# Kernel tuning notes

Measured on AMD Instinct MI355X. Metric: run time of the kernel, lower is better.

## Reference

```python
import jax, jax.numpy as jnp
import numpy as np

N_NODES = 100000
N_EDGES = 3200000
NUM_FEATURES = 1433
HIDDEN = 16
NUM_CLASSES = 7


def setup_inputs() -> dict:
    key = jax.random.key(0)
    k1, k2, k3, k4, k5, k6 = jax.random.split(key, 6)
    x = jax.random.normal(k1, (N_NODES, NUM_FEATURES), dtype=jnp.float32)
    edge_index = jax.random.randint(k2, (2, N_EDGES), 0, N_NODES, dtype=jnp.int64)
    # Glorot-ish init for the two GCN layer weights + zero biases
    W1 = jax.random.normal(k3, (NUM_FEATURES, HIDDEN), dtype=jnp.float32) / np.sqrt(NUM_FEATURES)
    b1 = jnp.zeros((HIDDEN,), dtype=jnp.float32)
    W2 = jax.random.normal(k4, (HIDDEN, NUM_CLASSES), dtype=jnp.float32) / np.sqrt(HIDDEN)
    b2 = jnp.zeros((NUM_CLASSES,), dtype=jnp.float32)
    return {"x": x, "edge_index": edge_index, "W1": W1, "b1": b1, "W2": W2, "b2": b2}


def _gcn_conv(x, W, b, src, dst, deg_inv_sqrt, n_nodes):
    # PyG GCNConv: h = D^{-1/2}(A+I)D^{-1/2} (x W) + b
    h = x @ W                                   # [N, out]
    coef = deg_inv_sqrt[src] * deg_inv_sqrt[dst]  # [E]
    msg = h[src] * coef[:, None]                # gather + scale, [E, out]
    agg = jax.ops.segment_sum(msg, dst, num_segments=n_nodes)  # scatter-add
    return agg + b


def reference(x, edge_index, W1, b1, W2, b2):
    n = x.shape[0]
    loops = jnp.arange(n, dtype=edge_index.dtype)
    src = jnp.concatenate([edge_index[0], loops])  # add self-loops
    dst = jnp.concatenate([edge_index[1], loops])
    deg = jax.ops.segment_sum(jnp.ones_like(dst, dtype=x.dtype), dst, num_segments=n)
    deg_inv_sqrt = jnp.where(deg > 0, jax.lax.rsqrt(deg), 0.0)

    h = _gcn_conv(x, W1, b1, src, dst, deg_inv_sqrt, n)
    h = jax.nn.relu(h)
    h = _gcn_conv(h, W2, b2, src, dst, deg_inv_sqrt, n)
    h = jax.nn.relu(h)
    return jax.nn.log_softmax(h, axis=1)
```

## Files before the change

### kernel.cpp

```cpp
#include <hip/hip_runtime.h>
#include <hip/hip_bf16.h>
#include <math.h>

#define NF 1433
#define NH 16
#define NC 7
#define NCH 45
#define NBKT_MAX 1024
#define SC_C 3072
#define CAP 4608
#define SMASK 0x1FFFFFFu

typedef __attribute__((ext_vector_type(8))) short bf16x8;
typedef __attribute__((ext_vector_type(4))) float f32x4;

__device__ __forceinline__ unsigned short f2bf(float f) {
  unsigned int u = __float_as_uint(f);
  unsigned int r = (u + 0x7FFFu + ((u >> 16) & 1u)) >> 16;
  return (unsigned short)r;
}
__device__ __forceinline__ short f2bfs(float f) {
  union { __hip_bfloat16 h; short s; } u;
  u.h = __float2bfloat16(f);
  return u.s;
}
__device__ __forceinline__ unsigned int packbf(float lo, float hi) {
  return (unsigned int)f2bf(lo) | ((unsigned int)f2bf(hi) << 16);
}
__device__ __forceinline__ void acc8(float* a, uint4 r) {
  a[0] += __uint_as_float(r.x << 16); a[1] += __uint_as_float(r.x & 0xffff0000u);
  a[2] += __uint_as_float(r.y << 16); a[3] += __uint_as_float(r.y & 0xffff0000u);
  a[4] += __uint_as_float(r.z << 16); a[5] += __uint_as_float(r.z & 0xffff0000u);
  a[6] += __uint_as_float(r.w << 16); a[7] += __uint_as_float(r.w & 0xffff0000u);
}
__device__ __forceinline__ void acc8f(float* a, uint4 r, float c) {
  a[0] = fmaf(__uint_as_float(r.x << 16), c, a[0]);
  a[1] = fmaf(__uint_as_float(r.x & 0xffff0000u), c, a[1]);
  a[2] = fmaf(__uint_as_float(r.y << 16), c, a[2]);
  a[3] = fmaf(__uint_as_float(r.y & 0xffff0000u), c, a[3]);
  a[4] = fmaf(__uint_as_float(r.z << 16), c, a[4]);
  a[5] = fmaf(__uint_as_float(r.z & 0xffff0000u), c, a[5]);
  a[6] = fmaf(__uint_as_float(r.w << 16), c, a[6]);
  a[7] = fmaf(__uint_as_float(r.w & 0xffff0000u), c, a[7]);
}

#define GLOAD(gp, lp) __builtin_amdgcn_global_load_lds(                     \
    (const __attribute__((address_space(1))) void*)(gp),                    \
    (__attribute__((address_space(3))) void*)(lp), 4, 0, 0)

__global__ void k_prep(const float* __restrict__ W1, short* __restrict__ Wb,
                       int* __restrict__ bfill) {
  int t = blockIdx.x * blockDim.x + threadIdx.x;
  if (t < NBKT_MAX) bfill[t * 16] = t * CAP;
  if (t >= NCH * 64 * 8) return;
  int i = t & 7, l = (t >> 3) & 63, c = t >> 9;
  int g = l >> 4, col = l & 15;
  int k = c * 32 + g * 8 + i;
  float v = (k < NF) ? W1[(size_t)k * NH + col] : 0.f;
  Wb[t] = (short)f2bf(v);
}

__global__ __launch_bounds__(256) void k_fused(
    const float* __restrict__ x, const short* __restrict__ Wb,
    const int* __restrict__ ei, int* __restrict__ bfill,
    int* __restrict__ ebuf, unsigned short* __restrict__ hs1,
    int n, int E, int nbkt, int nsb) {
  __shared__ __align__(16) char smem[49664];
  int blk = blockIdx.x, t = threadIdx.x;
  int q = blk / 7, r7 = blk % 7;
  bool is_scatter = (r7 == 0) && (q < nsb);

  if (is_scatter) {
    int* h   = (int*)smem;
    int* lo  = h + NBKT_MAX;
    int* lb  = lo + NBKT_MAX;
    int* wtot = lb + NBKT_MAX;
    int* sval = wtot + 8;
    unsigned short* sbkt = (unsigned short*)(sval + SC_C);
    const int* src = ei;
    const int* dst = ei + E;
    for (int i = t; i < NBKT_MAX; i += 256) h[i] = 0;
    __syncthreads();
    int e0 = q * SC_C;
    int e1 = min(E, e0 + SC_C);
    int csize = e1 - e0;
    for (int e = e0 + t; e < e1; e += 256)
      atomicAdd(&h[((unsigned)dst[e]) >> 7], 1);
    __syncthreads();
    {
      int lane = t & 63, wvq = t >> 6;
      int v0 = h[4 * t], v1 = h[4 * t + 1], v2 = h[4 * t + 2], v3 = h[4 * t + 3];
      int s4 = v0 + v1 + v2 + v3;
      int inc = s4;
#pragma unroll
      for (int o = 1; o < 64; o <<= 1) {
        int u = __shfl_up(inc, o, 64);
        if (lane >= o) inc += u;
      }
      if (lane == 63) wtot[wvq] = inc;
      __syncthreads();
      int wbase = 0;
#pragma unroll
      for (int wq = 0; wq < 4; ++wq) wbase += (wq < wvq) ? wtot[wq] : 0;
      int base = wbase + inc - s4;
      lo[4 * t]     = base;
      lo[4 * t + 1] = base + v0;
      lo[4 * t + 2] = base + v0 + v1;
      lo[4 * t + 3] = base + v0 + v1 + v2;
    }
    __syncthreads();
    for (int i = t; i < nbkt; i += 256) {
      int c = h[i];
      lb[i] = c ? atomicAdd(&bfill[i * 16], c) : 0;
      h[i] = 0;
    }
    __syncthreads();
    for (int e = e0 + t; e < e1; e += 256) {
      unsigned d = (unsigned)dst[e];
      int bk = d >> 7;
      int p = lo[bk] + atomicAdd(&h[bk], 1);
      sval[p] = (int)(((d & 127u) << 25) | (unsigned)src[e]);
      sbkt[p] = (unsigned short)bk;
    }
    __syncthreads();
    for (int i = t; i < csize; i += 256) {
      int bk = sbkt[i];
      ebuf[lb[bk] + (i - lo[bk])] = sval[i];
    }
    return;
  }

  int gemm_id = blk - min((blk + 6) / 7, nsb);
  float* xsf = (float*)smem;
#define XIDX(B, ROW, COL) ((((B) * 16 + (ROW)) * 388) + (COL))
  int l = t & 63, wv = t >> 6;
  int row0 = gemm_id << 4;
  int rl = l & 15, g = l >> 4;

  const bf16x8* wp = (const bf16x8*)Wb + l;
  f32x4 acc;
#pragma unroll
  for (int j = 0; j < 4; ++j) acc[j] = 0.f;

  const float* rp[4];
#pragma unroll
  for (int r = 0; r < 4; ++r) {
    int row = row0 + 4 * wv + r;
    rp[r] = x + (size_t)((row < n) ? row : (n - 1)) * NF;
  }

#define STAGE6(M0, B) do {                                                   \
    _Pragma("unroll") for (int r = 0; r < 4; ++r)                            \
    _Pragma("unroll") for (int j = 0; j < 6; ++j)                            \
      GLOAD(rp[r] + (M0) + j * 64 + l, xsf + XIDX(B, 4 * wv + r, j * 64));   \
  } while (0)

#define DOCHUNK(B, CC, WREG) do {                                            \
    const float4* p = (const float4*)(xsf + XIDX(B, rl, (CC) * 32 + g * 8)); \
    float4 a0 = p[0], a1 = p[1];                                             \
    bf16x8 af;                                                               \
    af[0] = f2bfs(a0.x); af[1] = f2bfs(a0.y);                                \
    af[2] = f2bfs(a0.z); af[3] = f2bfs(a0.w);                                \
    af[4] = f2bfs(a1.x); af[5] = f2bfs(a1.y);                                \
    af[6] = f2bfs(a1.z); af[7] = f2bfs(a1.w);                                \
    acc = __builtin_amdgcn_mfma_f32_16x16x32_bf16(af, WREG, acc, 0, 0, 0);   \
  } while (0)

  STAGE6(0, 0);
  bf16x8 w0 = wp[(size_t)(wv) * 64];
  bf16x8 w1 = wp[(size_t)(wv + 4) * 64];
  bf16x8 w2 = wp[(size_t)(wv + 8) * 64];
  STAGE6(384, 1);
  asm volatile("s_waitcnt vmcnt(24) lgkmcnt(0)" ::: "memory");
  __builtin_amdgcn_s_barrier();
  DOCHUNK(0, wv, w0); DOCHUNK(0, wv + 4, w1); DOCHUNK(0, wv + 8, w2);
  __builtin_amdgcn_s_barrier();
  w0 = wp[(size_t)(12 + wv) * 64];
  w1 = wp[(size_t)(16 + wv) * 64];
  w2 = wp[(size_t)(20 + wv) * 64];
  STAGE6(768, 0);
  asm volatile("s_waitcnt vmcnt(24) lgkmcnt(0)" ::: "memory");
  __builtin_amdgcn_s_barrier();
  DOCHUNK(1, wv, w0); DOCHUNK(1, wv + 4, w1); DOCHUNK(1, wv + 8, w2);
  __builtin_amdgcn_s_barrier();
  w0 = wp[(size_t)(24 + wv) * 64];
  w1 = wp[(size_t)(28 + wv) * 64];
  w2 = wp[(size_t)(32 + wv) * 64];
#pragma unroll
  for (int r = 0; r < 4; ++r) {
#pragma unroll
    for (int j = 0; j < 4; ++j)
      GLOAD(rp[r] + 1152 + j * 64 + l, xsf + XIDX(1, 4 * wv + r, j * 64));
    GLOAD(rp[r] + (NF - 64) + l, xsf + XIDX(1, 4 * wv + r, 217));
  }
  if (l < 28) xsf[XIDX(1, 4 * wv + (l / 7), 281 + (l % 7))] = 0.f;
  asm volatile("s_waitcnt vmcnt(20) lgkmcnt(0)" ::: "memory");
  __builtin_amdgcn_s_barrier();
  DOCHUNK(0, wv, w0); DOCHUNK(0, wv + 4, w1); DOCHUNK(0, wv + 8, w2);
  __builtin_amdgcn_s_barrier();
  w0 = wp[(size_t)(36 + wv) * 64];
  w1 = wp[(size_t)(40 + wv) * 64];
  bf16x8 w2b = wp[(size_t)44 * 64];
  asm volatile("s_waitcnt vmcnt(0) lgkmcnt(0)" ::: "memory");
  __builtin_amdgcn_s_barrier();
  DOCHUNK(1, wv, w0); DOCHUNK(1, wv + 4, w1);
  if (wv == 0) DOCHUNK(1, 8, w2b);
  __syncthreads();

  float* ps = xsf;
#pragma unroll
  for (int r = 0; r < 4; ++r)
    ps[(wv * 16 + g * 4 + r) * 16 + rl] = acc[r];
  __syncthreads();
  if (wv == 0) {
    int row = l >> 2, c0 = (l & 3) * 4;
    float4 s0 = *(const float4*)&ps[(row) * 16 + c0];
    float4 s1 = *(const float4*)&ps[(16 + row) * 16 + c0];
    float4 s2 = *(const float4*)&ps[(32 + row) * 16 + c0];
    float4 s3 = *(const float4*)&ps[(48 + row) * 16 + c0];
    int grow = row0 + row;
    if (grow < n) {
      ushort4 o;
      o.x = f2bf(s0.x + s1.x + s2.x + s3.x);
      o.y = f2bf(s0.y + s1.y + s2.y + s3.y);
      o.z = f2bf(s0.z + s1.z + s2.z + s3.z);
      o.w = f2bf(s0.w + s1.w + s2.w + s3.w);
      *(ushort4*)(hs1 + (size_t)grow * NH + c0) = o;
    }
  }
#undef STAGE6
#undef DOCHUNK
#undef XIDX
}

__global__ __launch_bounds__(256) void k_bcsr(const int* __restrict__ ebuf,
                                              const int* __restrict__ bfill,
                                              int* __restrict__ off,
                                              int* __restrict__ end,
                                              int* __restrict__ srcs,
                                              float* __restrict__ dis, int n) {
  __shared__ int s_in[CAP];
  __shared__ int s_out[CAP];
  __shared__ int s_cnt[256];
  __shared__ int s_sc[256];
  int b = blockIdx.x, t = threadIdx.x;
  int eb = b * CAP;
  int cnt = bfill[b * 16] - eb;
  int cnt4 = cnt >> 2;

  const int4* e4 = (const int4*)(ebuf + eb);
  for (int i = t; i < cnt4; i += 256) ((int4*)s_in)[i] = e4[i];
  for (int i = cnt4 * 4 + t; i < cnt; i += 256) s_in[i] = ebuf[eb + i];
  s_cnt[t] = 0;
  __syncthreads();
  for (int i = t; i < cnt; i += 256)
    atomicAdd(&s_cnt[((unsigned)s_in[i]) >> 25], 1);
  __syncthreads();
  int deg = s_cnt[t];
  s_sc[t] = deg;
  __syncthreads();
  for (int o = 1; o < 256; o <<= 1) {
    int u = (t >= o) ? s_sc[t - o] : 0;
    __syncthreads();
    s_sc[t] += u;
    __syncthreads();
  }
  int excl = s_sc[t] - deg;
  int node = (b << 7) + t;
  if (t < 128 && node < n) {
    off[node] = eb + excl;
    end[node] = eb + excl + deg;
    dis[node] = rsqrtf((float)deg + 1.0f);
  }
  __syncthreads();
  s_cnt[t] = excl;
  __syncthreads();
  for (int i = t; i < cnt; i += 256) {
    unsigned v = (unsigned)s_in[i];
    int slot = atomicAdd(&s_cnt[v >> 25], 1);
    s_out[slot] = (int)(v & SMASK);
  }
  __syncthreads();
  int4* sr4 = (int4*)(srcs + eb);
  for (int i = t; i < cnt4; i += 256) sr4[i] = ((int4*)s_out)[i];
  for (int i = cnt4 * 4 + t; i < cnt; i += 256) srcs[eb + i] = s_out[i];
}

__global__ __launch_bounds__(256) void k_pull1(
    const int* __restrict__ off, const int* __restrict__ end,
    const int* __restrict__ srcs, const float* __restrict__ dis,
    const uint4* __restrict__ hs1, const float* __restrict__ b1,
    const float* __restrict__ W2, uint4* __restrict__ hs2, int n) {
  int t = blockIdx.x * blockDim.x + threadIdx.x;
  int d = t >> 4;
  if (d >= n) return;
  int sub = t & 15, half = sub & 1, ph = sub >> 1;
  float dd = dis[d];

  float a[8] = {0.f, 0.f, 0.f, 0.f, 0.f, 0.f, 0.f, 0.f};
  if (ph == 0) acc8f(a, hs1[(size_t)d * 2 + half], dd);

  int k = off[d] + ph, k1 = end[d];
  for (; k + 8 < k1; k += 16) {
    int s0 = srcs[k], s1 = srcs[k + 8];
    float c0 = dis[s0], c1 = dis[s1];
    uint4 r0 = hs1[(size_t)s0 * 2 + half];
    uint4 r1 = hs1[(size_t)s1 * 2 + half];
    acc8f(a, r0, c0);
    acc8f(a, r1, c1);
  }
  if (k < k1) {
    int s = srcs[k];
    acc8f(a, hs1[(size_t)s * 2 + half], dis[s]);
  }

#pragma unroll
  for (int i = 0; i < 8; ++i) {
    a[i] += __shfl_xor(a[i], 2);
    a[i] += __shfl_xor(a[i], 4);
    a[i] += __shfl_xor(a[i], 8);
  }

  float v[8];
#pragma unroll
  for (int i = 0; i < 8; ++i) v[i] = fmaxf(a[i] * dd + b1[half * 8 + i], 0.f);
  float p[NC];
#pragma unroll
  for (int c = 0; c < NC; ++c) {
    float s = 0.f;
#pragma unroll
    for (int i = 0; i < 8; ++i) s = fmaf(v[i], W2[(half * 8 + i) * NC + c], s);
    p[c] = s;
  }
#pragma unroll
  for (int c = 0; c < NC; ++c) p[c] += __shfl_xor(p[c], 1);
  if (sub == 0) {
    uint4 o;
    o.x = packbf(p[0] * dd, p[1] * dd);
    o.y = packbf(p[2] * dd, p[3] * dd);
    o.z = packbf(p[4] * dd, p[5] * dd);
    o.w = packbf(p[6] * dd, 0.f);
    hs2[d] = o;
  }
}

__global__ __launch_bounds__(256) void k_pull2(
    const int* __restrict__ off, const int* __restrict__ end,
    const int* __restrict__ srcs, const float* __restrict__ dis,
    const uint4* __restrict__ hs2, const float* __restrict__ b2,
    float* __restrict__ out, int n) {
  int t = blockIdx.x * blockDim.x + threadIdx.x;
  int d = t >> 3;
  if (d >= n) return;
  int ph = t & 7;

  float a[8] = {0.f, 0.f, 0.f, 0.f, 0.f, 0.f, 0.f, 0.f};
  if (ph == 0) acc8(a, hs2[d]);

  int k = off[d] + ph, k1 = end[d];
  for (; k + 8 < k1; k += 16) {
    int s0 = srcs[k], s1 = srcs[k + 8];
    uint4 r0 = hs2[s0];
    uint4 r1 = hs2[s1];
    acc8(a, r0);
    acc8(a, r1);
  }
  if (k < k1) acc8(a, hs2[srcs[k]]);

#pragma unroll
  for (int i = 0; i < 8; ++i) {
    a[i] += __shfl_xor(a[i], 1);
    a[i] += __shfl_xor(a[i], 2);
    a[i] += __shfl_xor(a[i], 4);
  }
  float dd = dis[d];
  float u[NC];
#pragma unroll
  for (int c = 0; c < NC; ++c) u[c] = fmaxf(a[c] * dd + b2[c], 0.f);
  float m = u[0];
#pragma unroll
  for (int c = 1; c < NC; ++c) m = fmaxf(m, u[c]);
  float sum = 0.f;
#pragma unroll
  for (int c = 0; c < NC; ++c) sum += expf(u[c] - m);
  float lg = logf(sum);
  if (ph < NC) out[(size_t)d * NC + ph] = u[ph] - m - lg;
}

extern "C" void kernel_launch(void* const* d_in, const int* in_sizes, int n_in,
                              void* d_out, int out_size, void* d_ws, size_t ws_size,
                              hipStream_t stream) {
  const float* x  = (const float*)d_in[0];
  const int*   ei = (const int*)d_in[1];
  const float* W1 = (const float*)d_in[2];
  const float* b1 = (const float*)d_in[3];
  const float* W2 = (const float*)d_in[4];
  const float* b2 = (const float*)d_in[5];
  int n = in_sizes[0] / NF;
  int E = in_sizes[1] / 2;
  int nbkt = (n + 127) >> 7;

  char* w = (char*)d_ws;
#define TAKE(ptrty, name, bytes) \
  ptrty name = (ptrty)w; w += ((size_t)(bytes) + 15) & ~(size_t)15;
  TAKE(unsigned short*, hs1,  sizeof(short) * (size_t)n * NH)
  TAKE(uint4*,          hs2,  16 * (size_t)n)
  TAKE(float*,          dis,  sizeof(float) * n)
  TAKE(short*,          Wb,   sizeof(short) * NCH * 64 * 8)
  TAKE(int*,            bfill,sizeof(int) * 16 * NBKT_MAX)
  TAKE(int*,            ebuf, sizeof(int) * (size_t)NBKT_MAX * CAP)
  TAKE(int*,            off,  sizeof(int) * n)
  TAKE(int*,            end,  sizeof(int) * n)
  TAKE(int*,            srcs, sizeof(int) * (size_t)NBKT_MAX * CAP)
#undef TAKE
  float* out = (float*)d_out;

  int nsb = (E + SC_C - 1) / SC_C;
  int ntb = (n + 15) / 16;

  k_prep<<<(NCH * 64 * 8 + 255) / 256, 256, 0, stream>>>(W1, Wb, bfill);

  k_fused<<<nsb + ntb, 256, 0, stream>>>(x, Wb, ei, bfill, ebuf, hs1,
                                         n, E, nbkt, nsb);

  k_bcsr<<<nbkt, 256, 0, stream>>>(ebuf, bfill, off, end, srcs, dis, n);
  k_pull1<<<((size_t)n * 16 + 255) / 256, 256, 0, stream>>>(
      off, end, srcs, dis, (const uint4*)hs1, b1, W2, hs2, n);
  k_pull2<<<((size_t)n * 8 + 255) / 256, 256, 0, stream>>>(
      off, end, srcs, dis, hs2, b2, out, n);
}
```

Baseline: 235.9 us.

## Fuse bucket-CSR build into fused kernel with atomic completion counter

Moves the per-bucket CSR construction (k_bcsr) into trailing blocks of k_fused. Those blocks spin on a global done counter that each scatter block increments after writing its edges. The aim is to drop a kernel launch and let the CSR build overlap with the tail of the GEMM blocks. It relies on the scatter blocks being scheduled before the waiting blocks, which holds because of block ordering, and spinning blocks may hold CU slots while the GEMM is still running.

```diff
diff --git a/kernel.cpp b/kernel.cpp
--- a/kernel.cpp
+++ b/kernel.cpp
@@ -49,9 +49,10 @@
     (__attribute__((address_space(3))) void*)(lp), 4, 0, 0)
 
 __global__ void k_prep(const float* __restrict__ W1, short* __restrict__ Wb,
-                       int* __restrict__ bfill) {
+                       int* __restrict__ bfill, int* __restrict__ done) {
   int t = blockIdx.x * blockDim.x + threadIdx.x;
   if (t < NBKT_MAX) bfill[t * 16] = t * CAP;
+  if (t < 16) done[t] = 0;
   if (t >= NCH * 64 * 8) return;
   int i = t & 7, l = (t >> 3) & 63, c = t >> 9;
   int g = l >> 4, col = l & 15;
@@ -64,9 +65,67 @@
     const float* __restrict__ x, const short* __restrict__ Wb,
     const int* __restrict__ ei, int* __restrict__ bfill,
     int* __restrict__ ebuf, unsigned short* __restrict__ hs1,
-    int n, int E, int nbkt, int nsb) {
+    int* __restrict__ off, int* __restrict__ end, int* __restrict__ srcs,
+    float* __restrict__ dis, int* __restrict__ done,
+    int n, int E, int nbkt, int nsb, int ntb) {
   __shared__ __align__(16) char smem[49664];
   int blk = blockIdx.x, t = threadIdx.x;
+
+  if (blk >= nsb + ntb) {
+    int b = blk - nsb - ntb;
+    int* s_in  = (int*)smem;
+    int* s_out = s_in + CAP;
+    int* s_cnt = s_out + CAP;
+    int* s_sc  = s_cnt + 256;
+    if (t == 0) {
+      while (__hip_atomic_load(done, __ATOMIC_ACQUIRE,
+                               __HIP_MEMORY_SCOPE_AGENT) < nsb)
+        __builtin_amdgcn_s_sleep(32);
+    }
+    __syncthreads();
+
+    int eb = b * CAP;
+    int cnt = bfill[b * 16] - eb;
+    int cnt4 = cnt >> 2;
+    const int4* e4 = (const int4*)(ebuf + eb);
+    for (int i = t; i < cnt4; i += 256) ((int4*)s_in)[i] = e4[i];
+    for (int i = cnt4 * 4 + t; i < cnt; i += 256) s_in[i] = ebuf[eb + i];
+    s_cnt[t] = 0;
+    __syncthreads();
+    for (int i = t; i < cnt; i += 256)
+      atomicAdd(&s_cnt[((unsigned)s_in[i]) >> 25], 1);
+    __syncthreads();
+    int deg = s_cnt[t];
+    s_sc[t] = deg;
+    __syncthreads();
+    for (int o = 1; o < 256; o <<= 1) {
+      int u = (t >= o) ? s_sc[t - o] : 0;
+      __syncthreads();
+      s_sc[t] += u;
+      __syncthreads();
+    }
+    int excl = s_sc[t] - deg;
+    int node = (b << 7) + t;
+    if (t < 128 && node < n) {
+      off[node] = eb + excl;
+      end[node] = eb + excl + deg;
+      dis[node] = rsqrtf((float)deg + 1.0f);
+    }
+    __syncthreads();
+    s_cnt[t] = excl;
+    __syncthreads();
+    for (int i = t; i < cnt; i += 256) {
+      unsigned v = (unsigned)s_in[i];
+      int slot = atomicAdd(&s_cnt[v >> 25], 1);
+      s_out[slot] = (int)(v & SMASK);
+    }
+    __syncthreads();
+    int4* sr4 = (int4*)(srcs + eb);
+    for (int i = t; i < cnt4; i += 256) sr4[i] = ((int4*)s_out)[i];
+    for (int i = cnt4 * 4 + t; i < cnt; i += 256) srcs[eb + i] = s_out[i];
+    return;
+  }
+
   int q = blk / 7, r7 = blk % 7;
   bool is_scatter = (r7 == 0) && (q < nsb);
 
@@ -126,6 +185,12 @@
     for (int i = t; i < csize; i += 256) {
       int bk = sbkt[i];
       ebuf[lb[bk] + (i - lo[bk])] = sval[i];
+    }
+    __syncthreads();
+    if (t == 0) {
+      __threadfence();
+      __hip_atomic_fetch_add(done, 1, __ATOMIC_RELEASE,
+                             __HIP_MEMORY_SCOPE_AGENT);
     }
     return;
   }
@@ -233,59 +298,6 @@
 #undef XIDX
 }
 
-__global__ __launch_bounds__(256) void k_bcsr(const int* __restrict__ ebuf,
-                                              const int* __restrict__ bfill,
-                                              int* __restrict__ off,
-                                              int* __restrict__ end,
-                                              int* __restrict__ srcs,
-                                              float* __restrict__ dis, int n) {
-  __shared__ int s_in[CAP];
-  __shared__ int s_out[CAP];
-  __shared__ int s_cnt[256];
-  __shared__ int s_sc[256];
-  int b = blockIdx.x, t = threadIdx.x;
-  int eb = b * CAP;
-  int cnt = bfill[b * 16] - eb;
-  int cnt4 = cnt >> 2;
-
-  const int4* e4 = (const int4*)(ebuf + eb);
-  for (int i = t; i < cnt4; i += 256) ((int4*)s_in)[i] = e4[i];
-  for (int i = cnt4 * 4 + t; i < cnt; i += 256) s_in[i] = ebuf[eb + i];
-  s_cnt[t] = 0;
-  __syncthreads();
-  for (int i = t; i < cnt; i += 256)
-    atomicAdd(&s_cnt[((unsigned)s_in[i]) >> 25], 1);
-  __syncthreads();
-  int deg = s_cnt[t];
-  s_sc[t] = deg;
-  __syncthreads();
-  for (int o = 1; o < 256; o <<= 1) {
-    int u = (t >= o) ? s_sc[t - o] : 0;
-    __syncthreads();
-    s_sc[t] += u;
-    __syncthreads();
-  }
-  int excl = s_sc[t] - deg;
-  int node = (b << 7) + t;
-  if (t < 128 && node < n) {
-    off[node] = eb + excl;
-    end[node] = eb + excl + deg;
-    dis[node] = rsqrtf((float)deg + 1.0f);
-  }
-  __syncthreads();
-  s_cnt[t] = excl;
-  __syncthreads();
-  for (int i = t; i < cnt; i += 256) {
-    unsigned v = (unsigned)s_in[i];
-    int slot = atomicAdd(&s_cnt[v >> 25], 1);
-    s_out[slot] = (int)(v & SMASK);
-  }
-  __syncthreads();
-  int4* sr4 = (int4*)(srcs + eb);
-  for (int i = t; i < cnt4; i += 256) sr4[i] = ((int4*)s_out)[i];
-  for (int i = cnt4 * 4 + t; i < cnt; i += 256) srcs[eb + i] = s_out[i];
-}
-
 __global__ __launch_bounds__(256) void k_pull1(
     const int* __restrict__ off, const int* __restrict__ end,
     const int* __restrict__ srcs, const float* __restrict__ dis,
@@ -408,6 +420,7 @@
   TAKE(float*,          dis,  sizeof(float) * n)
   TAKE(short*,          Wb,   sizeof(short) * NCH * 64 * 8)
   TAKE(int*,            bfill,sizeof(int) * 16 * NBKT_MAX)
+  TAKE(int*,            done, sizeof(int) * 16)
   TAKE(int*,            ebuf, sizeof(int) * (size_t)NBKT_MAX * CAP)
   TAKE(int*,            off,  sizeof(int) * n)
   TAKE(int*,            end,  sizeof(int) * n)
@@ -418,12 +431,12 @@
   int nsb = (E + SC_C - 1) / SC_C;
   int ntb = (n + 15) / 16;
 
-  k_prep<<<(NCH * 64 * 8 + 255) / 256, 256, 0, stream>>>(W1, Wb, bfill);
-
-  k_fused<<<nsb + ntb, 256, 0, stream>>>(x, Wb, ei, bfill, ebuf, hs1,
-                                         n, E, nbkt, nsb);
-
-  k_bcsr<<<nbkt, 256, 0, stream>>>(ebuf, bfill, off, end, srcs, dis, n);
+  k_prep<<<(NCH * 64 * 8 + 255) / 256, 256, 0, stream>>>(W1, Wb, bfill, done);
+
+  k_fused<<<nsb + ntb + nbkt, 256, 0, stream>>>(
+      x, Wb, ei, bfill, ebuf, hs1, off, end, srcs, dis, done,
+      n, E, nbkt, nsb, ntb);
+
   k_pull1<<<((size_t)n * 16 + 255) / 256, 256, 0, stream>>>(
       off, end, srcs, dis, (const uint4*)hs1, b1, W2, hs2, n);
   k_pull2<<<((size_t)n * 8 + 255) / 256, 256, 0, stream>>>(
```

Result: slower. 425.5 us (+80.4%).

## Deepen GEMM staging pipeline and prescale layer-1 features by source degree

Applied to the files above, without the earlier changes.

The fused GEMM blocks now stage x in 256-column chunks through a double-buffered loop of five stages instead of 384-column chunks. This shrinks LDS from about 49 KB to 33 KB, which may allow more resident blocks and latency hiding. The CSR-building kernel now also multiplies each node's bf16 hidden row by its own deg^-1/2 after computing it. The layer-1 pull kernel can then sum neighbor rows directly without gathering dis[src] per edge. The cost is an extra read-modify-write of hs1 plus a second bf16 rounding of the scaled values.

```diff
diff --git a/kernel.cpp b/kernel.cpp
--- a/kernel.cpp
+++ b/kernel.cpp
@@ -33,20 +33,12 @@
   a[4] += __uint_as_float(r.z << 16); a[5] += __uint_as_float(r.z & 0xffff0000u);
   a[6] += __uint_as_float(r.w << 16); a[7] += __uint_as_float(r.w & 0xffff0000u);
 }
-__device__ __forceinline__ void acc8f(float* a, uint4 r, float c) {
-  a[0] = fmaf(__uint_as_float(r.x << 16), c, a[0]);
-  a[1] = fmaf(__uint_as_float(r.x & 0xffff0000u), c, a[1]);
-  a[2] = fmaf(__uint_as_float(r.y << 16), c, a[2]);
-  a[3] = fmaf(__uint_as_float(r.y & 0xffff0000u), c, a[3]);
-  a[4] = fmaf(__uint_as_float(r.z << 16), c, a[4]);
-  a[5] = fmaf(__uint_as_float(r.z & 0xffff0000u), c, a[5]);
-  a[6] = fmaf(__uint_as_float(r.w << 16), c, a[6]);
-  a[7] = fmaf(__uint_as_float(r.w & 0xffff0000u), c, a[7]);
-}
 
 #define GLOAD(gp, lp) __builtin_amdgcn_global_load_lds(                     \
     (const __attribute__((address_space(1))) void*)(gp),                    \
     (__attribute__((address_space(3))) void*)(lp), 4, 0, 0)
+
+#define SEP() asm volatile("" ::: "memory")
 
 __global__ void k_prep(const float* __restrict__ W1, short* __restrict__ Wb,
                        int* __restrict__ bfill) {
@@ -65,7 +57,7 @@
     const int* __restrict__ ei, int* __restrict__ bfill,
     int* __restrict__ ebuf, unsigned short* __restrict__ hs1,
     int n, int E, int nbkt, int nsb) {
-  __shared__ __align__(16) char smem[49664];
+  __shared__ __align__(16) char smem[33280];
   int blk = blockIdx.x, t = threadIdx.x;
   int q = blk / 7, r7 = blk % 7;
   bool is_scatter = (r7 == 0) && (q < nsb);
@@ -132,7 +124,7 @@
 
   int gemm_id = blk - min((blk + 6) / 7, nsb);
   float* xsf = (float*)smem;
-#define XIDX(B, ROW, COL) ((((B) * 16 + (ROW)) * 388) + (COL))
+#define XI(B, ROW, COL) ((((B) * 16 + (ROW)) * 260) + (COL))
   int l = t & 63, wv = t >> 6;
   int row0 = gemm_id << 4;
   int rl = l & 15, g = l >> 4;
@@ -149,14 +141,14 @@
     rp[r] = x + (size_t)((row < n) ? row : (n - 1)) * NF;
   }
 
-#define STAGE6(M0, B) do {                                                   \
+#define STAGEF(M0, B) do {                                                   \
     _Pragma("unroll") for (int r = 0; r < 4; ++r)                            \
-    _Pragma("unroll") for (int j = 0; j < 6; ++j)                            \
-      GLOAD(rp[r] + (M0) + j * 64 + l, xsf + XIDX(B, 4 * wv + r, j * 64));   \
+    _Pragma("unroll") for (int j = 0; j < 4; ++j)                            \
+      GLOAD(rp[r] + (M0) + j * 64 + l, xsf + XI(B, 4 * wv + r, j * 64));     \
   } while (0)
 
 #define DOCHUNK(B, CC, WREG) do {                                            \
-    const float4* p = (const float4*)(xsf + XIDX(B, rl, (CC) * 32 + g * 8)); \
+    const float4* p = (const float4*)(xsf + XI(B, rl, (CC) * 32 + g * 8));   \
     float4 a0 = p[0], a1 = p[1];                                             \
     bf16x8 af;                                                               \
     af[0] = f2bfs(a0.x); af[1] = f2bfs(a0.y);                                \
@@ -166,45 +158,57 @@
     acc = __builtin_amdgcn_mfma_f32_16x16x32_bf16(af, WREG, acc, 0, 0, 0);   \
   } while (0)
 
-  STAGE6(0, 0);
-  bf16x8 w0 = wp[(size_t)(wv) * 64];
-  bf16x8 w1 = wp[(size_t)(wv + 4) * 64];
-  bf16x8 w2 = wp[(size_t)(wv + 8) * 64];
-  STAGE6(384, 1);
-  asm volatile("s_waitcnt vmcnt(24) lgkmcnt(0)" ::: "memory");
+  bf16x8 w0 = wp[(size_t)(2 * wv) * 64];
+  bf16x8 w1 = wp[(size_t)(2 * wv + 1) * 64];
+  SEP();
+  STAGEF(0, 0);
+  SEP();
+  bf16x8 wn0 = wp[(size_t)(8 + 2 * wv) * 64];
+  bf16x8 wn1 = wp[(size_t)(9 + 2 * wv) * 64];
+  SEP();
+  STAGEF(256, 1);
+
+#pragma unroll
+  for (int m = 0; m < 4; ++m) {
+    asm volatile("s_waitcnt vmcnt(18) lgkmcnt(0)" ::: "memory");
+    __builtin_amdgcn_s_barrier();
+    DOCHUNK(m & 1, 2 * wv, w0);
+    DOCHUNK(m & 1, 2 * wv + 1, w1);
+    __builtin_amdgcn_s_barrier();
+    w0 = wn0; w1 = wn1;
+    if (m < 3) {
+      wn0 = wp[(size_t)(8 * (m + 2) + 2 * wv) * 64];
+      wn1 = wp[(size_t)(8 * (m + 2) + 2 * wv + 1) * 64];
+      SEP();
+      STAGEF(256 * (m + 2), m & 1);
+      SEP();
+    } else {
+      wn0 = wp[(size_t)(40 + wv) * 64];
+      wn1 = wp[(size_t)44 * 64];
+      SEP();
+#pragma unroll
+      for (int r = 0; r < 4; ++r) {
+#pragma unroll
+        for (int j = 0; j < 2; ++j)
+          GLOAD(rp[r] + 1280 + j * 64 + l, xsf + XI(1, 4 * wv + r, j * 64));
+        GLOAD(rp[r] + (NF - 64) + l, xsf + XI(1, 4 * wv + r, 89));
+      }
+      if (l < 28) xsf[XI(1, 4 * wv + (l / 7), 153 + (l % 7))] = 0.f;
+      SEP();
+    }
+  }
+
+  asm volatile("s_waitcnt vmcnt(14) lgkmcnt(0)" ::: "memory");
   __builtin_amdgcn_s_barrier();
-  DOCHUNK(0, wv, w0); DOCHUNK(0, wv + 4, w1); DOCHUNK(0, wv + 8, w2);
+  DOCHUNK(0, 2 * wv, w0);
+  DOCHUNK(0, 2 * wv + 1, w1);
   __builtin_amdgcn_s_barrier();
-  w0 = wp[(size_t)(12 + wv) * 64];
-  w1 = wp[(size_t)(16 + wv) * 64];
-  w2 = wp[(size_t)(20 + wv) * 64];
-  STAGE6(768, 0);
-  asm volatile("s_waitcnt vmcnt(24) lgkmcnt(0)" ::: "memory");
-  __builtin_amdgcn_s_barrier();
-  DOCHUNK(1, wv, w0); DOCHUNK(1, wv + 4, w1); DOCHUNK(1, wv + 8, w2);
-  __builtin_amdgcn_s_barrier();
-  w0 = wp[(size_t)(24 + wv) * 64];
-  w1 = wp[(size_t)(28 + wv) * 64];
-  w2 = wp[(size_t)(32 + wv) * 64];
-#pragma unroll
-  for (int r = 0; r < 4; ++r) {
-#pragma unroll
-    for (int j = 0; j < 4; ++j)
-      GLOAD(rp[r] + 1152 + j * 64 + l, xsf + XIDX(1, 4 * wv + r, j * 64));
-    GLOAD(rp[r] + (NF - 64) + l, xsf + XIDX(1, 4 * wv + r, 217));
-  }
-  if (l < 28) xsf[XIDX(1, 4 * wv + (l / 7), 281 + (l % 7))] = 0.f;
-  asm volatile("s_waitcnt vmcnt(20) lgkmcnt(0)" ::: "memory");
-  __builtin_amdgcn_s_barrier();
-  DOCHUNK(0, wv, w0); DOCHUNK(0, wv + 4, w1); DOCHUNK(0, wv + 8, w2);
-  __builtin_amdgcn_s_barrier();
-  w0 = wp[(size_t)(36 + wv) * 64];
-  w1 = wp[(size_t)(40 + wv) * 64];
-  bf16x8 w2b = wp[(size_t)44 * 64];
+  w0 = wn0; w1 = wn1;
+
   asm volatile("s_waitcnt vmcnt(0) lgkmcnt(0)" ::: "memory");
   __builtin_amdgcn_s_barrier();
-  DOCHUNK(1, wv, w0); DOCHUNK(1, wv + 4, w1);
-  if (wv == 0) DOCHUNK(1, 8, w2b);
+  DOCHUNK(1, wv, w0);
+  if (wv == 0) DOCHUNK(1, 4, w1);
   __syncthreads();
 
   float* ps = xsf;
@@ -228,9 +232,9 @@
       *(ushort4*)(hs1 + (size_t)grow * NH + c0) = o;
     }
   }
-#undef STAGE6
+#undef STAGEF
 #undef DOCHUNK
-#undef XIDX
+#undef XI
 }
 
 __global__ __launch_bounds__(256) void k_bcsr(const int* __restrict__ ebuf,
@@ -238,11 +242,14 @@
                                               int* __restrict__ off,
                                               int* __restrict__ end,
                                               int* __restrict__ srcs,
-                                              float* __restrict__ dis, int n) {
+                                              float* __restrict__ dis,
+                                              unsigned short* __restrict__ hs1,
+                                              int n) {
   __shared__ int s_in[CAP];
   __shared__ int s_out[CAP];
   __shared__ int s_cnt[256];
   __shared__ int s_sc[256];
+  __shared__ float s_dis[128];
   int b = blockIdx.x, t = threadIdx.x;
   int eb = b * CAP;
   int cnt = bfill[b * 16] - eb;
@@ -268,9 +275,11 @@
   int excl = s_sc[t] - deg;
   int node = (b << 7) + t;
   if (t < 128 && node < n) {
+    float dd = rsqrtf((float)deg + 1.0f);
     off[node] = eb + excl;
     end[node] = eb + excl + deg;
-    dis[node] = rsqrtf((float)deg + 1.0f);
+    dis[node] = dd;
+    s_dis[t] = dd;
   }
   __syncthreads();
   s_cnt[t] = excl;
@@ -284,6 +293,26 @@
   int4* sr4 = (int4*)(srcs + eb);
   for (int i = t; i < cnt4; i += 256) sr4[i] = ((int4*)s_out)[i];
   for (int i = cnt4 * 4 + t; i < cnt; i += 256) srcs[eb + i] = s_out[i];
+
+  {
+    int nl = t >> 1, hf = t & 1;
+    int nd = (b << 7) + nl;
+    if (nd < n) {
+      float dd = s_dis[nl];
+      uint4* hp = (uint4*)hs1 + (size_t)nd * 2 + hf;
+      uint4 r = *hp;
+      uint4 o;
+      o.x = packbf(__uint_as_float(r.x << 16) * dd,
+                   __uint_as_float(r.x & 0xffff0000u) * dd);
+      o.y = packbf(__uint_as_float(r.y << 16) * dd,
+                   __uint_as_float(r.y & 0xffff0000u) * dd);
+      o.z = packbf(__uint_as_float(r.z << 16) * dd,
+                   __uint_as_float(r.z & 0xffff0000u) * dd);
+      o.w = packbf(__uint_as_float(r.w << 16) * dd,
+                   __uint_as_float(r.w & 0xffff0000u) * dd);
+      *hp = o;
+    }
+  }
 }
 
 __global__ __launch_bounds__(256) void k_pull1(
@@ -295,24 +324,19 @@
   int d = t >> 4;
   if (d >= n) return;
   int sub = t & 15, half = sub & 1, ph = sub >> 1;
-  float dd = dis[d];
 
   float a[8] = {0.f, 0.f, 0.f, 0.f, 0.f, 0.f, 0.f, 0.f};
-  if (ph == 0) acc8f(a, hs1[(size_t)d * 2 + half], dd);
+  if (ph == 0) acc8(a, hs1[(size_t)d * 2 + half]);
 
   int k = off[d] + ph, k1 = end[d];
   for (; k + 8 < k1; k += 16) {
     int s0 = srcs[k], s1 = srcs[k + 8];
-    float c0 = dis[s0], c1 = dis[s1];
     uint4 r0 = hs1[(size_t)s0 * 2 + half];
     uint4 r1 = hs1[(size_t)s1 * 2 + half];
-    acc8f(a, r0, c0);
-    acc8f(a, r1, c1);
-  }
-  if (k < k1) {
-    int s = srcs[k];
-    acc8f(a, hs1[(size_t)s * 2 + half], dis[s]);
-  }
+    acc8(a, r0);
+    acc8(a, r1);
+  }
+  if (k < k1) acc8(a, hs1[(size_t)srcs[k] * 2 + half]);
 
 #pragma unroll
   for (int i = 0; i < 8; ++i) {
@@ -321,6 +345,7 @@
     a[i] += __shfl_xor(a[i], 8);
   }
 
+  float dd = dis[d];
   float v[8];
 #pragma unroll
   for (int i = 0; i < 8; ++i) v[i] = fmaxf(a[i] * dd + b1[half * 8 + i], 0.f);
@@ -423,7 +448,7 @@
   k_fused<<<nsb + ntb, 256, 0, stream>>>(x, Wb, ei, bfill, ebuf, hs1,
                                          n, E, nbkt, nsb);
 
-  k_bcsr<<<nbkt, 256, 0, stream>>>(ebuf, bfill, off, end, srcs, dis, n);
+  k_bcsr<<<nbkt, 256, 0, stream>>>(ebuf, bfill, off, end, srcs, dis, hs1, n);
   k_pull1<<<((size_t)n * 16 + 255) / 256, 256, 0, stream>>>(
       off, end, srcs, dis, (const uint4*)hs1, b1, W2, hs2, n);
   k_pull2<<<((size_t)n * 8 + 255) / 256, 256, 0, stream>>>(
```

Measured after the change: 219.2 us. 7.1% less time.
